# Kernel optimization log

Measured on AMD Instinct MI355X. Metric: run time of the kernel, lower is better.

## Reference

```python
import jax, jax.numpy as jnp
import numpy as np

B, S, H = 1, 1024, 2048
NH, HD = 16, 128
E, K, FI, SFI = 8, 2, 1408, 2816
EPS = 1e-6
THETA = 10000.0


def setup_inputs() -> dict:
    key = jax.random.key(0)
    ks = jax.random.split(key, 14)
    sc = 0.02
    return {
        "hidden_states": jax.random.normal(ks[0], (B, S, H), jnp.float32),
        "ln1_w": jnp.ones((H,), jnp.float32),
        "ln2_w": jnp.ones((H,), jnp.float32),
        "wq": jax.random.normal(ks[1], (H, H), jnp.float32) * sc,
        "wk": jax.random.normal(ks[2], (H, H), jnp.float32) * sc,
        "wv": jax.random.normal(ks[3], (H, H), jnp.float32) * sc,
        "wo": jax.random.normal(ks[4], (H, H), jnp.float32) * sc,
        "gate_w": jax.random.normal(ks[5], (E, H), jnp.float32) * sc,
        "expert_gate": jax.random.normal(ks[6], (E, FI, H), jnp.float32) * sc,
        "expert_up": jax.random.normal(ks[7], (E, FI, H), jnp.float32) * sc,
        "expert_down": jax.random.normal(ks[8], (E, H, FI), jnp.float32) * sc,
        "shared_gate": jax.random.normal(ks[9], (SFI, H), jnp.float32) * sc,
        "shared_up": jax.random.normal(ks[10], (SFI, H), jnp.float32) * sc,
        "shared_down": jax.random.normal(ks[11], (H, SFI), jnp.float32) * sc,
    }


def _rmsnorm(x, w):
    v = jnp.mean(x * x, axis=-1, keepdims=True)
    return x * jax.lax.rsqrt(v + EPS) * w


def _rotate_half(x):
    x1, x2 = x[..., : HD // 2], x[..., HD // 2 :]
    return jnp.concatenate((-x2, x1), axis=-1)


def _rope_cos_sin():
    inv_freq = 1.0 / (THETA ** (jnp.arange(0, HD, 2, dtype=jnp.float32) / HD))
    t = jnp.arange(S, dtype=jnp.float32)
    freqs = t[:, None] * inv_freq[None, :]          # [S, HD//2]
    emb = jnp.concatenate((freqs, freqs), axis=-1)  # [S, HD]
    return jnp.cos(emb)[None, None], jnp.sin(emb)[None, None]  # [1,1,S,HD]


def _decoder_layer(hidden_states, ln1_w, ln2_w, wq, wk, wv, wo, gate_w,
                   expert_gate, expert_up, expert_down,
                   shared_gate, shared_up, shared_down):
    # ---- self-attention ----
    residual = hidden_states
    h = _rmsnorm(hidden_states, ln1_w)
    q = (h @ wq.T).reshape(B, S, NH, HD).transpose(0, 2, 1, 3)  # [B,NH,S,HD]
    k = (h @ wk.T).reshape(B, S, NH, HD).transpose(0, 2, 1, 3)
    v = (h @ wv.T).reshape(B, S, NH, HD).transpose(0, 2, 1, 3)
    cos, sin = _rope_cos_sin()
    q = q * cos + _rotate_half(q) * sin
    k = k * cos + _rotate_half(k) * sin
    scores = jnp.einsum('bhqd,bhkd->bhqk', q, k) / jnp.sqrt(jnp.float32(HD))
    causal = jnp.tril(jnp.ones((S, S), bool))
    scores = jnp.where(causal[None, None], scores, jnp.finfo(jnp.float32).min)
    probs = jax.nn.softmax(scores, axis=-1)
    attn = jnp.einsum('bhqk,bhkd->bhqd', probs, v)
    attn = attn.transpose(0, 2, 1, 3).reshape(B, S, H)
    x = residual + attn @ wo.T

    # ---- MoE MLP ----
    residual = x
    h2 = _rmsnorm(x, ln2_w)
    flat = h2.reshape(-1, H)                       # [N,H], N=B*S
    n_tok = flat.shape[0]
    logits = flat @ gate_w.T                       # [N,E]
    gate_scores = jax.nn.softmax(logits, axis=-1)
    topk_w, topk_idx = jax.lax.top_k(gate_scores, K)
    topk_w = topk_w / (jnp.sum(topk_w, axis=-1, keepdims=True) + 1e-20)
    # dense combine weights [N,E] (zero for unrouted experts)
    combine = jnp.zeros((n_tok, E), flat.dtype).at[
        jnp.arange(n_tok)[:, None], topk_idx].add(topk_w)
    # SwiGLU per expert, dense over all experts, then weighted combine
    g = jnp.einsum('nh,efh->enf', flat, expert_gate)   # [E,N,FI]
    u = jnp.einsum('nh,efh->enf', flat, expert_up)
    act = jax.nn.silu(g) * u
    eo = jnp.einsum('enf,ehf->enh', act, expert_down)  # [E,N,H]
    routed = jnp.einsum('enh,ne->nh', eo, combine)
    # shared experts (always on)
    shared = (jax.nn.silu(flat @ shared_gate.T) * (flat @ shared_up.T)) @ shared_down.T
    return residual + (routed + shared).reshape(B, S, H)


def reference(hidden_states, ln1_w, ln2_w, wq, wk, wv, wo, gate_w,
              expert_gate, expert_up, expert_down,
              shared_gate, shared_up, shared_down):
    return _decoder_layer(hidden_states, ln1_w, ln2_w, wq, wk, wv, wo, gate_w,
                          expert_gate, expert_up, expert_down,
                          shared_gate, shared_up, shared_down)
```

## Files before the change

kernel.cpp:

```cpp
#include <hip/hip_runtime.h>
#include <hip/hip_bf16.h>


#define DI __device__ __forceinline__

typedef __attribute__((ext_vector_type(8))) short short8;
typedef __attribute__((ext_vector_type(4))) float f32x4;
using u16 = unsigned short;

struct alignas(8) U16x4 { u16 x, y, z, w; };

DI u16 f2bf(float f) {
  unsigned u = __float_as_uint(f);
  u += 0x7fffu + ((u >> 16) & 1u);
  return (u16)(u >> 16);
}
DI float bf2f(u16 h) { return __uint_as_float(((unsigned)h) << 16); }

DI void gload16(const void* g, void* l) {
  __builtin_amdgcn_global_load_lds((const __attribute__((address_space(1))) void*)g,
                                   (__attribute__((address_space(3))) void*)l, 16, 0, 0);
}


__global__ __launch_bounds__(256) void k_ropetab(float* __restrict__ tab) {
  int idx = blockIdx.x * 256 + threadIdx.x;
  int s = idx >> 6, i = idx & 63;
  double inv = pow(10000.0, -(double)(2 * i) / 128.0);
  double ang = (double)s * inv;
  tab[idx * 2 + 0] = (float)cos(ang);
  tab[idx * 2 + 1] = (float)sin(ang);
}

__global__ __launch_bounds__(256) void k_rmsnorm(const float* __restrict__ in,
                                                 const float* __restrict__ w,
                                                 float* __restrict__ outf,
                                                 u16* __restrict__ outh,
                                                 u16* __restrict__ outl) {
  const int row = blockIdx.x, t = threadIdx.x;
  const float* x = in + (size_t)row * 2048;
  float4 a = *(const float4*)&x[t * 4];
  float4 b = *(const float4*)&x[1024 + t * 4];
  float ss = a.x * a.x + a.y * a.y + a.z * a.z + a.w * a.w +
             b.x * b.x + b.y * b.y + b.z * b.z + b.w * b.w;
#pragma unroll
  for (int off = 32; off; off >>= 1) ss += __shfl_xor(ss, off);
  __shared__ float red[4];
  if ((t & 63) == 0) red[t >> 6] = ss;
  __syncthreads();
  float total = red[0] + red[1] + red[2] + red[3];
  float r = 1.0f / sqrtf(total * (1.0f / 2048.0f) + 1e-6f);
  float4 wa = *(const float4*)&w[t * 4];
  float4 wb = *(const float4*)&w[1024 + t * 4];
  float va[8] = {a.x * r * wa.x, a.y * r * wa.y, a.z * r * wa.z, a.w * r * wa.w,
                 b.x * r * wb.x, b.y * r * wb.y, b.z * r * wb.z, b.w * r * wb.w};
  if (outf) {
    *(float4*)&outf[(size_t)row * 2048 + t * 4] = make_float4(va[0], va[1], va[2], va[3]);
    *(float4*)&outf[(size_t)row * 2048 + 1024 + t * 4] = make_float4(va[4], va[5], va[6], va[7]);
  }
  if (outh) {
    U16x4 ha{f2bf(va[0]), f2bf(va[1]), f2bf(va[2]), f2bf(va[3])};
    U16x4 hb{f2bf(va[4]), f2bf(va[5]), f2bf(va[6]), f2bf(va[7])};
    *(U16x4*)&outh[(size_t)row * 2048 + t * 4] = ha;
    *(U16x4*)&outh[(size_t)row * 2048 + 1024 + t * 4] = hb;
    if (outl) {
      U16x4 la{f2bf(va[0] - bf2f(ha.x)), f2bf(va[1] - bf2f(ha.y)),
               f2bf(va[2] - bf2f(ha.z)), f2bf(va[3] - bf2f(ha.w))};
      U16x4 lb{f2bf(va[4] - bf2f(hb.x)), f2bf(va[5] - bf2f(hb.y)),
               f2bf(va[6] - bf2f(hb.z)), f2bf(va[7] - bf2f(hb.w))};
      *(U16x4*)&outl[(size_t)row * 2048 + t * 4] = la;
      *(U16x4*)&outl[(size_t)row * 2048 + 1024 + t * 4] = lb;
    }
  }
}

__global__ __launch_bounds__(256) void k_splitf(const float* __restrict__ src,
                                                u16* __restrict__ dh,
                                                u16* __restrict__ dl) {
  int idx = (blockIdx.x * 256 + threadIdx.x) * 4;
  float4 v = *(const float4*)&src[idx];
  U16x4 h{f2bf(v.x), f2bf(v.y), f2bf(v.z), f2bf(v.w)};
  U16x4 l{f2bf(v.x - bf2f(h.x)), f2bf(v.y - bf2f(h.y)),
          f2bf(v.z - bf2f(h.z)), f2bf(v.w - bf2f(h.w))};
  *(U16x4*)&dh[idx] = h;
  *(U16x4*)&dl[idx] = l;
}

__global__ __launch_bounds__(256) void k_rope(float* __restrict__ q, float* __restrict__ k,
                                              const float* __restrict__ tab) {
  int idx = blockIdx.x * 256 + threadIdx.x;
  int s = idx >> 10, rem = idx & 1023;
  int h = rem >> 6, i = rem & 63;
  size_t base = (size_t)s * 2048 + h * 128 + i;
  float c = tab[(s * 64 + i) * 2 + 0];
  float sn = tab[(s * 64 + i) * 2 + 1];
  const float qs = 0.08838834764831845f;
  float q1 = q[base], q2 = q[base + 64];
  q[base] = (q1 * c - q2 * sn) * qs;
  q[base + 64] = (q2 * c + q1 * sn) * qs;
  float k1 = k[base], k2 = k[base + 64];
  k[base] = k1 * c - k2 * sn;
  k[base + 64] = k2 * c + k1 * sn;
}

__global__ __launch_bounds__(256) void k_splitkv(
    const float* __restrict__ qf, const float* __restrict__ kf,
    const float* __restrict__ vf,
    u16* __restrict__ Qh, u16* __restrict__ Ql,
    u16* __restrict__ Kh, u16* __restrict__ Kl,
    u16* __restrict__ Vth, u16* __restrict__ Vtl) {
  int idx = (blockIdx.x * 256 + threadIdx.x) * 4;
  int s = idx >> 11, c = idx & 2047;
  float4 q4 = *(const float4*)&qf[idx];
  U16x4 qh{f2bf(q4.x), f2bf(q4.y), f2bf(q4.z), f2bf(q4.w)};
  U16x4 ql{f2bf(q4.x - bf2f(qh.x)), f2bf(q4.y - bf2f(qh.y)),
           f2bf(q4.z - bf2f(qh.z)), f2bf(q4.w - bf2f(qh.w))};
  *(U16x4*)&Qh[idx] = qh; *(U16x4*)&Ql[idx] = ql;
  float4 k4 = *(const float4*)&kf[idx];
  U16x4 kh{f2bf(k4.x), f2bf(k4.y), f2bf(k4.z), f2bf(k4.w)};
  U16x4 kl{f2bf(k4.x - bf2f(kh.x)), f2bf(k4.y - bf2f(kh.y)),
           f2bf(k4.z - bf2f(kh.z)), f2bf(k4.w - bf2f(kh.w))};
  *(U16x4*)&Kh[idx] = kh; *(U16x4*)&Kl[idx] = kl;
  float4 v4 = *(const float4*)&vf[idx];
  float vv[4] = {v4.x, v4.y, v4.z, v4.w};
#pragma unroll
  for (int i = 0; i < 4; ++i) {
    u16 hv = f2bf(vv[i]);
    u16 lv = f2bf(vv[i] - bf2f(hv));
    Vth[(size_t)(c + i) * 1024 + s] = hv;
    Vtl[(size_t)(c + i) * 1024 + s] = lv;
  }
}

DI void stage_kv(const u16* __restrict__ Khg, const u16* __restrict__ Klg,
                 const u16* __restrict__ Vhg, const u16* __restrict__ Vlg,
                 u16* lsKh, u16* lsKl, u16* lsVh, u16* lsVl,
                 int kvb, int hh, int wv, int lane) {
#pragma unroll
  for (int it = 0; it < 4; ++it) {
    const int ebase = it * 2048 + wv * 512;
    const int eo = ebase + lane * 8;
    {
      const int rr = eo >> 7, cg = (eo >> 3) & 15;
      const size_t src = (size_t)(kvb + rr) * 2048 + hh * 128 + ((cg ^ (rr & 7)) << 3);
      gload16(Khg + src, lsKh + ebase);
      gload16(Klg + src, lsKl + ebase);
    }
    {
      const int rr = eo >> 6, cg = (eo >> 3) & 7;
      const size_t src = (size_t)(hh * 128 + rr) * 1024 + kvb + ((cg ^ (rr & 7)) << 3);
      gload16(Vhg + src, lsVh + ebase);
      gload16(Vlg + src, lsVl + ebase);
    }
  }
}

__global__ __launch_bounds__(256) void k_attn_tile(
    const u16* __restrict__ Qh, const u16* __restrict__ Ql,
    const u16* __restrict__ Khg, const u16* __restrict__ Klg,
    const u16* __restrict__ Vhg, const u16* __restrict__ Vlg,
    u16* __restrict__ atth, u16* __restrict__ attl) {
  __shared__ u16 lsKh[2][8192], lsKl[2][8192], lsVh[2][8192], lsVl[2][8192];
  __shared__ u16 Plh[4][16][72], Pll[4][16][72];
  const int hh = blockIdx.y;
  const int qb = blockIdx.x * 64;
  const int tid = threadIdx.x, lane = tid & 63, wv = tid >> 6;
  const int l15 = lane & 15, grp = lane >> 4;
  u16(*plh)[72] = Plh[wv];
  u16(*pll)[72] = Pll[wv];
  const int q_glob = qb + wv * 16 + l15;
  const int tend = blockIdx.x + 1;

  short8 qfh[4], qfl[4];
  const size_t qbase = (size_t)q_glob * 2048 + hh * 128;
#pragma unroll
  for (int c = 0; c < 4; ++c) {
    qfh[c] = *(const short8*)&Qh[qbase + c * 32 + grp * 8];
    qfl[c] = *(const short8*)&Ql[qbase + c * 32 + grp * 8];
  }
  f32x4 oacc[8];
#pragma unroll
  for (int dc = 0; dc < 8; ++dc) oacc[dc] = 0.f;
  float m_run = -1e30f, l_run = 0.f;

  int cur = 0;
  stage_kv(Khg, Klg, Vhg, Vlg, lsKh[0], lsKl[0], lsVh[0], lsVl[0], 0, hh, wv, lane);
  __syncthreads();

  for (int kt = 0; kt < tend; ++kt) {
    const int kvb = kt * 64;
    if (kt + 1 < tend)
      stage_kv(Khg, Klg, Vhg, Vlg, lsKh[cur ^ 1], lsKl[cur ^ 1], lsVh[cur ^ 1],
               lsVl[cur ^ 1], kvb + 64, hh, wv, lane);
    const u16* kh = lsKh[cur];
    const u16* kl = lsKl[cur];
    const u16* vh = lsVh[cur];
    const u16* vl = lsVl[cur];

    f32x4 s4[4];
#pragma unroll
    for (int sub = 0; sub < 4; ++sub) {
      f32x4 a = {0.f, 0.f, 0.f, 0.f};
      const int kr = sub * 16 + l15;
      const int sw = kr & 7;
#pragma unroll
      for (int c = 0; c < 4; ++c) {
        const int off = kr * 128 + ((((c << 2) | grp) ^ sw) << 3);
        short8 khf = *(const short8*)&kh[off];
        short8 klf = *(const short8*)&kl[off];
        a = __builtin_amdgcn_mfma_f32_16x16x32_bf16(khf, qfh[c], a, 0, 0, 0);
        a = __builtin_amdgcn_mfma_f32_16x16x32_bf16(klf, qfh[c], a, 0, 0, 0);
        a = __builtin_amdgcn_mfma_f32_16x16x32_bf16(khf, qfl[c], a, 0, 0, 0);
      }
      s4[sub] = a;
    }
    if (kt == tend - 1) {
#pragma unroll
      for (int sub = 0; sub < 4; ++sub)
#pragma unroll
        for (int r = 0; r < 4; ++r) {
          int kv = kvb + sub * 16 + grp * 4 + r;
          if (kv > q_glob) s4[sub][r] = -1e30f;
        }
    }
    float tmax = s4[0][0];
#pragma unroll
    for (int sub = 0; sub < 4; ++sub)
#pragma unroll
      for (int r = 0; r < 4; ++r) tmax = fmaxf(tmax, s4[sub][r]);
    tmax = fmaxf(tmax, __shfl_xor(tmax, 16));
    tmax = fmaxf(tmax, __shfl_xor(tmax, 32));
    float mnew = fmaxf(m_run, tmax);
    float scale = expf(m_run - mnew);
    float p[16], lsum = 0.f;
#pragma unroll
    for (int sub = 0; sub < 4; ++sub)
#pragma unroll
      for (int r = 0; r < 4; ++r) {
        float pe = expf(s4[sub][r] - mnew);
        p[sub * 4 + r] = pe;
        lsum += pe;
      }
    lsum += __shfl_xor(lsum, 16);
    lsum += __shfl_xor(lsum, 32);
    l_run = l_run * scale + lsum;
    m_run = mnew;
#pragma unroll
    for (int dc = 0; dc < 8; ++dc) oacc[dc] *= scale;
#pragma unroll
    for (int sub = 0; sub < 4; ++sub)
#pragma unroll
      for (int rp = 0; rp < 2; ++rp) {
        int i0 = sub * 4 + rp * 2;
        u16 h0 = f2bf(p[i0]), h1 = f2bf(p[i0 + 1]);
        u16 lo0 = f2bf(p[i0] - bf2f(h0)), lo1 = f2bf(p[i0 + 1] - bf2f(h1));
        int kvoff = sub * 16 + grp * 4 + rp * 2;
        *(unsigned*)&plh[l15][kvoff] = (unsigned)h0 | ((unsigned)h1 << 16);
        *(unsigned*)&pll[l15][kvoff] = (unsigned)lo0 | ((unsigned)lo1 << 16);
      }
    short8 phf[2], plf[2];
#pragma unroll
    for (int ks = 0; ks < 2; ++ks) {
      phf[ks] = *(const short8*)&plh[l15][ks * 32 + grp * 8];
      plf[ks] = *(const short8*)&pll[l15][ks * 32 + grp * 8];
    }
#pragma unroll
    for (int dc = 0; dc < 8; ++dc) {
      const int dr = dc * 16 + l15;
      const int sw = dr & 7;
      f32x4 acc = oacc[dc];
#pragma unroll
      for (int ks = 0; ks < 2; ++ks) {
        const int voff = dr * 64 + ((((ks << 2) | grp) ^ sw) << 3);
        short8 vhf = *(const short8*)&vh[voff];
        short8 vlf = *(const short8*)&vl[voff];
        acc = __builtin_amdgcn_mfma_f32_16x16x32_bf16(vhf, phf[ks], acc, 0, 0, 0);
        acc = __builtin_amdgcn_mfma_f32_16x16x32_bf16(vlf, phf[ks], acc, 0, 0, 0);
        acc = __builtin_amdgcn_mfma_f32_16x16x32_bf16(vhf, plf[ks], acc, 0, 0, 0);
      }
      oacc[dc] = acc;
    }
    __syncthreads();
    cur ^= 1;
  }
  float inv = 1.0f / l_run;
#pragma unroll
  for (int dc = 0; dc < 8; ++dc)
#pragma unroll
    for (int rp = 0; rp < 2; ++rp) {
      float v0 = oacc[dc][rp * 2] * inv;
      float v1 = oacc[dc][rp * 2 + 1] * inv;
      u16 h0 = f2bf(v0), h1 = f2bf(v1);
      u16 lo0 = f2bf(v0 - bf2f(h0)), lo1 = f2bf(v1 - bf2f(h1));
      size_t o = (size_t)q_glob * 2048 + hh * 128 + dc * 16 + grp * 4 + rp * 2;
      *(unsigned*)&atth[o] = (unsigned)h0 | ((unsigned)h1 << 16);
      *(unsigned*)&attl[o] = (unsigned)lo0 | ((unsigned)lo1 << 16);
    }
}

__global__ __launch_bounds__(256) void k_router(const float* __restrict__ h2f,
                                                const float* __restrict__ gw,
                                                int2* __restrict__ tidx,
                                                float2* __restrict__ twgt) {
  const int tok = blockIdx.x;
  const float* hrow = h2f + (size_t)tok * 2048;
  float part[8];
#pragma unroll
  for (int e = 0; e < 8; ++e) part[e] = 0.f;
  for (int j = 0; j < 8; ++j) {
    int p = j * 256 + threadIdx.x;
    float hv = hrow[p];
#pragma unroll
    for (int e = 0; e < 8; ++e) part[e] += hv * gw[e * 2048 + p];
  }
#pragma unroll
  for (int e = 0; e < 8; ++e)
#pragma unroll
    for (int off = 32; off; off >>= 1) part[e] += __shfl_xor(part[e], off);
  __shared__ float red[4][8];
  int wv = threadIdx.x >> 6, lane = threadIdx.x & 63;
  if (lane == 0) {
#pragma unroll
    for (int e = 0; e < 8; ++e) red[wv][e] = part[e];
  }
  __syncthreads();
  if (threadIdx.x == 0) {
    float lg[8];
#pragma unroll
    for (int e = 0; e < 8; ++e) lg[e] = red[0][e] + red[1][e] + red[2][e] + red[3][e];
    float m = lg[0];
#pragma unroll
    for (int e = 1; e < 8; ++e) m = fmaxf(m, lg[e]);
    float ex[8], s = 0.f;
#pragma unroll
    for (int e = 0; e < 8; ++e) { ex[e] = expf(lg[e] - m); s += ex[e]; }
#pragma unroll
    for (int e = 0; e < 8; ++e) ex[e] /= s;
    int i1 = 0;
#pragma unroll
    for (int e = 1; e < 8; ++e) if (ex[e] > ex[i1]) i1 = e;
    int i2 = (i1 == 0) ? 1 : 0;
#pragma unroll
    for (int e = 0; e < 8; ++e) if (e != i1 && ex[e] > ex[i2]) i2 = e;
    float s2 = ex[i1] + ex[i2] + 1e-20f;
    tidx[tok] = make_int2(i1, i2);
    twgt[tok] = make_float2(ex[i1] / s2, ex[i2] / s2);
  }
}

__global__ __launch_bounds__(64) void k_scan(const int2* __restrict__ tidx,
                                             const float2* __restrict__ twgt,
                                             int* __restrict__ meta,
                                             int* __restrict__ toklist,
                                             float* __restrict__ slotw,
                                             int* __restrict__ slots) {
  const int lane = threadIdx.x;
  int base = 0;
  for (int e = 0; e < 8; ++e) {
    int cnt = 0;
    for (int c = 0; c < 16; ++c) {
      const int tok = c * 64 + lane;
      int2 my = tidx[tok];
      int f1 = (my.x == e), f2 = (my.y == e);
      int flag = f1 | f2;
      unsigned long long m = __ballot(flag);
      if (flag) {
        float2 w = twgt[tok];
        int rank = (int)__popcll(m & ((1ull << lane) - 1ull));
        int s = base + cnt + rank;
        toklist[s] = tok;
        slotw[s] = f1 ? w.x : w.y;
        slots[tok * 2 + (f1 ? 0 : 1)] = s;
      }
      cnt += (int)__popcll(m);
    }
    if (lane == 0) { meta[e] = base; meta[9 + e] = cnt; }
    const int padded = ((cnt + 127) >> 7) << 7;
    for (int s = cnt + lane; s < padded; s += 64) {
      toklist[base + s] = 0;
      slotw[base + s] = 0.f;
    }
    base += padded;
  }
  if (lane == 0) meta[8] = base;
}


DI void stageA_bf16(const u16* __restrict__ A, size_t lda, int row0, int k0,
                    u16* lsA, int tid) {
  const int lane = tid & 63, wv = tid >> 6;
#pragma unroll
  for (int it = 0; it < 2; ++it) {
    const int ebase = it * 2048 + wv * 512;
    const int eo = ebase + lane * 8;
    const int rr = eo >> 5, cc = eo & 31;
    gload16(A + (size_t)(row0 + rr) * lda + k0 + cc, lsA + ebase);
  }
}
template <int NJ>
DI void loadB_regs(const float* __restrict__ B, size_t ldb, int row0, int k0,
                   int tid, float4* r) {
#pragma unroll
  for (int j = 0; j < NJ; ++j) {
    const int eo = (j * 256 + tid) * 4;
    const int rr = eo >> 5, cc = eo & 31;
    r[j] = *(const float4*)(B + (size_t)(row0 + rr) * ldb + k0 + cc);
  }
}
template <int NJ>
DI void writeB_lds(u16* lsB, int tid, const float4* r) {
#pragma unroll
  for (int j = 0; j < NJ; ++j) {
    const int eo = (j * 256 + tid) * 4;
    U16x4 hv{f2bf(r[j].x), f2bf(r[j].y), f2bf(r[j].z), f2bf(r[j].w)};
    *(U16x4*)&lsB[eo] = hv;
  }
}

__global__ __launch_bounds__(256) void k_gemm_bf16split(
    const u16* __restrict__ Ah, const u16* __restrict__ Al,
    const u16* __restrict__ Bh0, const u16* __restrict__ Bl0,
    const u16* __restrict__ Bh1, const u16* __restrict__ Bl1,
    const u16* __restrict__ Bh2, const u16* __restrict__ Bl2,
    float* __restrict__ C0, float* __restrict__ C1, float* __restrict__ C2,
    const float* __restrict__ resid) {
  __shared__ u16 lsAh[4096], lsAl[4096], lsBh[4096], lsBl[4096];
  const int z = blockIdx.z;
  const u16* Bh = (z == 0) ? Bh0 : (z == 1) ? Bh1 : Bh2;
  const u16* Bl = (z == 0) ? Bl0 : (z == 1) ? Bl1 : Bl2;
  float* Cm = (z == 0) ? C0 : (z == 1) ? C1 : C2;
  const int tid = threadIdx.x, lane = tid & 63, wv = tid >> 6;
  const int wr = (wv >> 1) * 64, wc = (wv & 1) * 64;
  const int fr = lane & 15, fg = lane >> 4;
  const int row0 = blockIdx.x * 128, col0 = blockIdx.y * 128;
  f32x4 acc[4][4];
#pragma unroll
  for (int i = 0; i < 4; ++i)
#pragma unroll
    for (int j = 0; j < 4; ++j) acc[i][j] = 0.f;

  for (int kt = 0; kt < 64; ++kt) {
    const int k0 = kt * 32;
    stageA_bf16(Ah, 2048, row0, k0, lsAh, tid);
    stageA_bf16(Al, 2048, row0, k0, lsAl, tid);
    stageA_bf16(Bh, 2048, col0, k0, lsBh, tid);
    stageA_bf16(Bl, 2048, col0, k0, lsBl, tid);
    __syncthreads();
    short8 ah[4], al[4], bh[4], bl[4];
#pragma unroll
    for (int mi = 0; mi < 4; ++mi) {
      const int off = (wr + mi * 16 + fr) * 32 + fg * 8;
      ah[mi] = *(const short8*)&lsAh[off];
      al[mi] = *(const short8*)&lsAl[off];
    }
#pragma unroll
    for (int ni = 0; ni < 4; ++ni) {
      const int off = (wc + ni * 16 + fr) * 32 + fg * 8;
      bh[ni] = *(const short8*)&lsBh[off];
      bl[ni] = *(const short8*)&lsBl[off];
    }
#pragma unroll
    for (int mi = 0; mi < 4; ++mi)
#pragma unroll
      for (int ni = 0; ni < 4; ++ni) {
        f32x4 c = acc[mi][ni];
        c = __builtin_amdgcn_mfma_f32_16x16x32_bf16(al[mi], bh[ni], c, 0, 0, 0);
        c = __builtin_amdgcn_mfma_f32_16x16x32_bf16(ah[mi], bl[ni], c, 0, 0, 0);
        c = __builtin_amdgcn_mfma_f32_16x16x32_bf16(ah[mi], bh[ni], c, 0, 0, 0);
        acc[mi][ni] = c;
      }
    __syncthreads();
  }
  const bool hasres = (resid != nullptr);
#pragma unroll
  for (int mi = 0; mi < 4; ++mi)
#pragma unroll
    for (int ni = 0; ni < 4; ++ni)
#pragma unroll
      for (int qq = 0; qq < 4; ++qq) {
        const int row = row0 + wr + mi * 16 + fg * 4 + qq;
        const int col = col0 + wc + ni * 16 + fr;
        float val = acc[mi][ni][qq];
        if (hasres) val += resid[(size_t)row * 2048 + col];
        Cm[(size_t)row * 2048 + col] = val;
      }
}

DI int tile_to_expert(const int* meta, int t) {
  int e = 0;
  while (e < 7 && t >= (meta[e + 1] >> 7)) ++e;
  return e;
}

__global__ __launch_bounds__(256) void k_dual_all(
    const u16* __restrict__ h2b, const float* __restrict__ eg,
    const float* __restrict__ eu, const float* __restrict__ sg,
    const float* __restrict__ su, const int* __restrict__ meta,
    const int* __restrict__ toklist, const float* __restrict__ slotw,
    u16* __restrict__ act, u16* __restrict__ acts) {
  const int bid = blockIdx.x;
  const bool isShared = bid >= 528;
  __shared__ int toks[128];
  __shared__ u16 lsA[2][4096], lsG[2][2048], lsU[2][2048];
  const int tid = threadIdx.x, lane = tid & 63, wv = tid >> 6;
  const int wr = (wv >> 1) * 64, wc = (wv & 1) * 32;
  const int fr = lane & 15, fg = lane >> 4;

  int n0, e = 0, off_e = 0, cnt_e = 0, rtile = 0;
  const float *Bg, *Bu;
  if (isShared) {
    const int b2 = bid - 528;
    rtile = b2 / 44;
    n0 = (b2 % 44) * 64;
    Bg = sg;
    Bu = su;
    if (tid < 128) toks[tid] = rtile * 128 + tid;
  } else {
    const int t = bid / 22;
    if (t >= (meta[8] >> 7)) return;
    n0 = (bid % 22) * 64;
    e = tile_to_expert(meta, t);
    off_e = meta[e];
    cnt_e = meta[9 + e];
    rtile = t - (off_e >> 7);
    Bg = eg + (size_t)e * 1408 * 2048;
    Bu = eu + (size_t)e * 1408 * 2048;
    if (tid < 128) toks[tid] = toklist[off_e + rtile * 128 + tid] & 1023;
  }
  f32x4 ag[4][2], au[4][2];
#pragma unroll
  for (int i = 0; i < 4; ++i)
#pragma unroll
    for (int j = 0; j < 2; ++j) { ag[i][j] = 0.f; au[i][j] = 0.f; }
  __syncthreads();

  auto stageAg = [&](u16* dst, int k0) {
#pragma unroll
    for (int it = 0; it < 2; ++it) {
      const int ebase = it * 2048 + wv * 512;
      const int eo = ebase + lane * 8;
      const int rr = eo >> 5, cc = eo & 31;
      gload16(h2b + (size_t)toks[rr] * 2048 + k0 + cc, dst + ebase);
    }
  };

  float4 gpre[2], upre[2];
  stageAg(lsA[0], 0);
  loadB_regs<2>(Bg, 2048, n0, 0, tid, gpre);
  loadB_regs<2>(Bu, 2048, n0, 0, tid, upre);
  writeB_lds<2>(lsG[0], tid, gpre);
  writeB_lds<2>(lsU[0], tid, upre);
  __syncthreads();

  int cur = 0;
  for (int kt = 0; kt < 64; ++kt) {
    const int k1 = (kt + 1) * 32;
    const bool pf = (kt + 1 < 64);
    if (pf) {
      stageAg(lsA[cur ^ 1], k1);
      loadB_regs<2>(Bg, 2048, n0, k1, tid, gpre);
      loadB_regs<2>(Bu, 2048, n0, k1, tid, upre);
    }
    short8 af[4], gf[2], uf[2];
#pragma unroll
    for (int mi = 0; mi < 4; ++mi)
      af[mi] = *(const short8*)&lsA[cur][(wr + mi * 16 + fr) * 32 + fg * 8];
#pragma unroll
    for (int ni = 0; ni < 2; ++ni) {
      const int off = (wc + ni * 16 + fr) * 32 + fg * 8;
      gf[ni] = *(const short8*)&lsG[cur][off];
      uf[ni] = *(const short8*)&lsU[cur][off];
    }
#pragma unroll
    for (int mi = 0; mi < 4; ++mi)
#pragma unroll
      for (int ni = 0; ni < 2; ++ni) {
        ag[mi][ni] = __builtin_amdgcn_mfma_f32_16x16x32_bf16(af[mi], gf[ni], ag[mi][ni], 0, 0, 0);
        au[mi][ni] = __builtin_amdgcn_mfma_f32_16x16x32_bf16(af[mi], uf[ni], au[mi][ni], 0, 0, 0);
      }
    if (pf) {
      writeB_lds<2>(lsG[cur ^ 1], tid, gpre);
      writeB_lds<2>(lsU[cur ^ 1], tid, upre);
    }
    __syncthreads();
    cur ^= 1;
  }
#pragma unroll
  for (int mi = 0; mi < 4; ++mi)
#pragma unroll
    for (int ni = 0; ni < 2; ++ni)
#pragma unroll
      for (int qq = 0; qq < 4; ++qq) {
        const int r = wr + mi * 16 + fg * 4 + qq;
        const int col = n0 + wc + ni * 16 + fr;
        float g = ag[mi][ni][qq], u = au[mi][ni][qq];
        float a = g / (1.0f + expf(-g)) * u;
        if (isShared) {
          acts[(size_t)(rtile * 128 + r) * 2816 + col] = f2bf(a);
        } else {
          const int rowInE = rtile * 128 + r;
          if (rowInE < cnt_e)
            act[(size_t)(off_e + rowInE) * 1408 + col] = f2bf(a * slotw[off_e + rowInE]);
        }
      }
}

__global__ __launch_bounds__(256) void k_down_all(
    const u16* __restrict__ act, const float* __restrict__ ed,
    const u16* __restrict__ acts, const float* __restrict__ sd,
    const int* __restrict__ meta, float* __restrict__ dwn,
    float* __restrict__ shd) {
  __shared__ u16 lsA[2][4096], lsB[2][4096];
  const int bid = blockIdx.x;
  const int tid = threadIdx.x, lane = tid & 63, wv = tid >> 6;
  const int fr = lane & 15, fg = lane >> 4;
  if (bid < 384) {
    const int t = bid >> 4;
    if (t >= (meta[8] >> 7)) return;
    const int col0 = (bid & 15) * 128;
    const int e = tile_to_expert(meta, t);
    const int off_e = meta[e];
    const int rtile = t - (off_e >> 7);
    const int wr = (wv >> 1) * 64, wc = (wv & 1) * 64;
    const u16* Ab = act + (size_t)off_e * 1408;
    const float* Bb = ed + (size_t)e * 2048 * 1408;
    f32x4 acc[4][4];
#pragma unroll
    for (int i = 0; i < 4; ++i)
#pragma unroll
      for (int j = 0; j < 4; ++j) acc[i][j] = 0.f;
    float4 bpre[4];
    stageA_bf16(Ab, 1408, rtile * 128, 0, lsA[0], tid);
    loadB_regs<4>(Bb, 1408, col0, 0, tid, bpre);
    writeB_lds<4>(lsB[0], tid, bpre);
    __syncthreads();
    int cur = 0;
    for (int kt = 0; kt < 44; ++kt) {
      const int k1 = (kt + 1) * 32;
      const bool pf = (kt + 1 < 44);
      if (pf) {
        stageA_bf16(Ab, 1408, rtile * 128, k1, lsA[cur ^ 1], tid);
        loadB_regs<4>(Bb, 1408, col0, k1, tid, bpre);
      }
      short8 af[4], bf_[4];
#pragma unroll
      for (int mi = 0; mi < 4; ++mi)
        af[mi] = *(const short8*)&lsA[cur][(wr + mi * 16 + fr) * 32 + fg * 8];
#pragma unroll
      for (int ni = 0; ni < 4; ++ni)
        bf_[ni] = *(const short8*)&lsB[cur][(wc + ni * 16 + fr) * 32 + fg * 8];
#pragma unroll
      for (int mi = 0; mi < 4; ++mi)
#pragma unroll
        for (int ni = 0; ni < 4; ++ni)
          acc[mi][ni] = __builtin_amdgcn_mfma_f32_16x16x32_bf16(af[mi], bf_[ni], acc[mi][ni], 0, 0, 0);
      if (pf) writeB_lds<4>(lsB[cur ^ 1], tid, bpre);
      __syncthreads();
      cur ^= 1;
    }
#pragma unroll
    for (int mi = 0; mi < 4; ++mi)
#pragma unroll
      for (int ni = 0; ni < 4; ++ni)
#pragma unroll
        for (int qq = 0; qq < 4; ++qq) {
          const int r = wr + mi * 16 + fg * 4 + qq;
          const int col = col0 + wc + ni * 16 + fr;
          dwn[(size_t)(off_e + rtile * 128 + r) * 2048 + col] = acc[mi][ni][qq];
        }
  } else {
    const int b2 = bid - 384;
    const int row0 = (b2 >> 5) * 128;
    const int col0 = (b2 & 31) * 64;
    const int wr = (wv >> 1) * 64, wc = (wv & 1) * 32;
    f32x4 acc[4][2];
#pragma unroll
    for (int i = 0; i < 4; ++i)
#pragma unroll
      for (int j = 0; j < 2; ++j) acc[i][j] = 0.f;
    float4 bpre[2];
    stageA_bf16(acts, 2816, row0, 0, lsA[0], tid);
    loadB_regs<2>(sd, 2816, col0, 0, tid, bpre);
    writeB_lds<2>(lsB[0], tid, bpre);
    __syncthreads();
    int cur = 0;
    for (int kt = 0; kt < 88; ++kt) {
      const int k1 = (kt + 1) * 32;
      const bool pf = (kt + 1 < 88);
      if (pf) {
        stageA_bf16(acts, 2816, row0, k1, lsA[cur ^ 1], tid);
        loadB_regs<2>(sd, 2816, col0, k1, tid, bpre);
      }
      short8 af[4], bf_[2];
#pragma unroll
      for (int mi = 0; mi < 4; ++mi)
        af[mi] = *(const short8*)&lsA[cur][(wr + mi * 16 + fr) * 32 + fg * 8];
#pragma unroll
      for (int ni = 0; ni < 2; ++ni)
        bf_[ni] = *(const short8*)&lsB[cur][(wc + ni * 16 + fr) * 32 + fg * 8];
#pragma unroll
      for (int mi = 0; mi < 4; ++mi)
#pragma unroll
        for (int ni = 0; ni < 2; ++ni)
          acc[mi][ni] = __builtin_amdgcn_mfma_f32_16x16x32_bf16(af[mi], bf_[ni], acc[mi][ni], 0, 0, 0);
      if (pf) writeB_lds<2>(lsB[cur ^ 1], tid, bpre);
      __syncthreads();
      cur ^= 1;
    }
#pragma unroll
    for (int mi = 0; mi < 4; ++mi)
#pragma unroll
      for (int ni = 0; ni < 2; ++ni)
#pragma unroll
        for (int qq = 0; qq < 4; ++qq) {
          const int row = row0 + wr + mi * 16 + fg * 4 + qq;
          const int col = col0 + wc + ni * 16 + fr;
          shd[(size_t)row * 2048 + col] = acc[mi][ni][qq];
        }
  }
}

__global__ __launch_bounds__(256) void k_combine(
    const float* __restrict__ shd, const float* __restrict__ x,
    const float* __restrict__ dwn, const int* __restrict__ slots,
    float* __restrict__ outp) {
  const int i4 = (blockIdx.x * 256 + threadIdx.x) * 4;
  const int row = i4 >> 11, col = i4 & 2047;
  const int s0 = slots[row * 2], s1 = slots[row * 2 + 1];
  float4 a = *(const float4*)&shd[i4];
  float4 b = *(const float4*)&x[i4];
  float4 c = *(const float4*)&dwn[(size_t)s0 * 2048 + col];
  float4 d = *(const float4*)&dwn[(size_t)s1 * 2048 + col];
  float4 o;
  o.x = a.x + b.x + c.x + d.x;
  o.y = a.y + b.y + c.y + d.y;
  o.z = a.z + b.z + c.z + d.z;
  o.w = a.w + b.w + c.w + d.w;
  *(float4*)&outp[i4] = o;
}


extern "C" void kernel_launch(void* const* d_in, const int* in_sizes, int n_in,
                              void* d_out, int out_size, void* d_ws, size_t ws_size,
                              hipStream_t stream) {
  (void)in_sizes; (void)n_in; (void)out_size; (void)ws_size;
  const float* hidden = (const float*)d_in[0];
  const float* ln1 = (const float*)d_in[1];
  const float* ln2 = (const float*)d_in[2];
  const float* wq = (const float*)d_in[3];
  const float* wk = (const float*)d_in[4];
  const float* wvw = (const float*)d_in[5];
  const float* wo = (const float*)d_in[6];
  const float* gw = (const float*)d_in[7];
  const float* eg = (const float*)d_in[8];
  const float* eu = (const float*)d_in[9];
  const float* ed = (const float*)d_in[10];
  const float* sg = (const float*)d_in[11];
  const float* su = (const float*)d_in[12];
  const float* sd = (const float*)d_in[13];
  float* out = (float*)d_out;
  char* ws = (char*)d_ws;

  const size_t KB = 1ull << 10, MB = 1ull << 20;
  float* tab = (float*)(ws + 0);
  int2* tidx = (int2*)(ws + 512 * KB);
  float2* twgt = (float2*)(ws + 520 * KB);
  int* meta = (int*)(ws + 528 * KB);
  int* tokl = (int*)(ws + 532 * KB);
  float* slw = (float*)(ws + 544 * KB);
  int* slots = (int*)(ws + 556 * KB);
  u16* hnh = (u16*)(ws + 1 * MB);
  u16* hnl = (u16*)(ws + 5 * MB);
  u16* wqh = (u16*)(ws + 9 * MB);
  u16* wql = (u16*)(ws + 17 * MB);
  u16* wkh = (u16*)(ws + 25 * MB);
  u16* wkl = (u16*)(ws + 33 * MB);
  u16* wvh = (u16*)(ws + 41 * MB);
  u16* wvl = (u16*)(ws + 49 * MB);
  u16* woh = (u16*)(ws + 57 * MB);
  u16* wol = (u16*)(ws + 65 * MB);
  float* qf = (float*)(ws + 73 * MB);
  float* kf = (float*)(ws + 81 * MB);
  float* vf = (float*)(ws + 89 * MB);
  u16* Qh = (u16*)(ws + 9 * MB);
  u16* Ql = (u16*)(ws + 13 * MB);
  u16* Kh = (u16*)(ws + 17 * MB);
  u16* Kl = (u16*)(ws + 21 * MB);
  u16* Vth = (u16*)(ws + 25 * MB);
  u16* Vtl = (u16*)(ws + 29 * MB);
  u16* atth = (u16*)(ws + 33 * MB);
  u16* attl = (u16*)(ws + 37 * MB);
  float* xf = (float*)(ws + 41 * MB);
  float* h2f = (float*)(ws + 49 * MB);
  u16* h2b = (u16*)(ws + 1 * MB);
  u16* act = (u16*)(ws + 73 * MB);
  u16* acts = (u16*)(ws + 82 * MB);
  float* dwn = (float*)(ws + 9 * MB);
  float* shd = (float*)(ws + 33 * MB);

  k_ropetab<<<256, 256, 0, stream>>>(tab);
  k_rmsnorm<<<1024, 256, 0, stream>>>(hidden, ln1, nullptr, hnh, hnl);
  k_splitf<<<4096, 256, 0, stream>>>(wq, wqh, wql);
  k_splitf<<<4096, 256, 0, stream>>>(wk, wkh, wkl);
  k_splitf<<<4096, 256, 0, stream>>>(wvw, wvh, wvl);
  k_splitf<<<4096, 256, 0, stream>>>(wo, woh, wol);
  k_gemm_bf16split<<<dim3(8, 16, 3), 256, 0, stream>>>(
      hnh, hnl, wqh, wql, wkh, wkl, wvh, wvl, qf, kf, vf, nullptr);
  k_rope<<<4096, 256, 0, stream>>>(qf, kf, tab);
  k_splitkv<<<2048, 256, 0, stream>>>(qf, kf, vf, Qh, Ql, Kh, Kl, Vth, Vtl);
  k_attn_tile<<<dim3(16, 16), 256, 0, stream>>>(Qh, Ql, Kh, Kl, Vth, Vtl, atth, attl);
  k_gemm_bf16split<<<dim3(8, 16, 1), 256, 0, stream>>>(
      atth, attl, woh, wol, woh, wol, woh, wol, xf, xf, xf, hidden);
  k_rmsnorm<<<1024, 256, 0, stream>>>(xf, ln2, h2f, h2b, nullptr);
  k_router<<<1024, 256, 0, stream>>>(h2f, gw, tidx, twgt);
  k_scan<<<1, 64, 0, stream>>>(tidx, twgt, meta, tokl, slw, slots);
  k_dual_all<<<880, 256, 0, stream>>>(h2b, eg, eu, sg, su, meta, tokl, slw, act, acts);
  k_down_all<<<640, 256, 0, stream>>>(act, ed, acts, sd, meta, dwn, shd);
  k_combine<<<2048, 256, 0, stream>>>(shd, xf, dwn, slots, out);
}
```

Measured before the change: 590.1 us.

## Remap MoE GEMM block order for XCD locality, hoist addresses, merge weight splits

Block indices in the expert gate/up and down kernels are remapped so that each group of blocks (blockIdx mod 8, likely meant to match the XCDs) works on the same weight columns across row tiles. This is meant to improve L2 reuse of the fp32 weight streams. Per-iteration address arithmetic is hoisted into precomputed pointers. The bf16 conversion of weight tiles now uses a cheaper round-half-up pack that drops round-to-nearest-even, so results can differ slightly. The four weight-split launches are merged into one kernel.

Result: slower. 635.8 us (+7.7%).

```diff
diff --git a/kernel.cpp b/kernel.cpp
--- a/kernel.cpp
+++ b/kernel.cpp
@@ -16,6 +16,11 @@
   return (u16)(u >> 16);
 }
 DI float bf2f(u16 h) { return __uint_as_float(((unsigned)h) << 16); }
+DI unsigned pack2(float f0, float f1) {
+  unsigned a = __float_as_uint(f0) + 0x8000u;
+  unsigned b = __float_as_uint(f1) + 0x8000u;
+  return (a >> 16) | (b & 0xffff0000u);
+}
 
 DI void gload16(const void* g, void* l) {
   __builtin_amdgcn_global_load_lds((const __attribute__((address_space(1))) void*)g,
@@ -74,10 +79,17 @@
   }
 }
 
-__global__ __launch_bounds__(256) void k_splitf(const float* __restrict__ src,
-                                                u16* __restrict__ dh,
-                                                u16* __restrict__ dl) {
-  int idx = (blockIdx.x * 256 + threadIdx.x) * 4;
+__global__ __launch_bounds__(256) void k_splitf4(
+    const float* __restrict__ s0, const float* __restrict__ s1,
+    const float* __restrict__ s2, const float* __restrict__ s3,
+    u16* __restrict__ h0, u16* __restrict__ h1, u16* __restrict__ h2,
+    u16* __restrict__ h3, u16* __restrict__ l0, u16* __restrict__ l1,
+    u16* __restrict__ l2, u16* __restrict__ l3) {
+  const int which = blockIdx.x >> 12;
+  const int idx = ((blockIdx.x & 4095) * 256 + threadIdx.x) * 4;
+  const float* src = (which == 0) ? s0 : (which == 1) ? s1 : (which == 2) ? s2 : s3;
+  u16* dh = (which == 0) ? h0 : (which == 1) ? h1 : (which == 2) ? h2 : h3;
+  u16* dl = (which == 0) ? l0 : (which == 1) ? l1 : (which == 2) ? l2 : l3;
   float4 v = *(const float4*)&src[idx];
   U16x4 h{f2bf(v.x), f2bf(v.y), f2bf(v.z), f2bf(v.w)};
   U16x4 l{f2bf(v.x - bf2f(h.x)), f2bf(v.y - bf2f(h.y)),
@@ -397,25 +409,6 @@
     gload16(A + (size_t)(row0 + rr) * lda + k0 + cc, lsA + ebase);
   }
 }
-template <int NJ>
-DI void loadB_regs(const float* __restrict__ B, size_t ldb, int row0, int k0,
-                   int tid, float4* r) {
-#pragma unroll
-  for (int j = 0; j < NJ; ++j) {
-    const int eo = (j * 256 + tid) * 4;
-    const int rr = eo >> 5, cc = eo & 31;
-    r[j] = *(const float4*)(B + (size_t)(row0 + rr) * ldb + k0 + cc);
-  }
-}
-template <int NJ>
-DI void writeB_lds(u16* lsB, int tid, const float4* r) {
-#pragma unroll
-  for (int j = 0; j < NJ; ++j) {
-    const int eo = (j * 256 + tid) * 4;
-    U16x4 hv{f2bf(r[j].x), f2bf(r[j].y), f2bf(r[j].z), f2bf(r[j].w)};
-    *(U16x4*)&lsB[eo] = hv;
-  }
-}
 
 __global__ __launch_bounds__(256) void k_gemm_bf16split(
     const u16* __restrict__ Ah, const u16* __restrict__ Al,
@@ -498,28 +491,28 @@
     const float* __restrict__ su, const int* __restrict__ meta,
     const int* __restrict__ toklist, const float* __restrict__ slotw,
     u16* __restrict__ act, u16* __restrict__ acts) {
-  const int bid = blockIdx.x;
-  const bool isShared = bid >= 528;
+  const int wid = ((blockIdx.x & 7) * 110) + (blockIdx.x >> 3);
+  const bool isShared = wid >= 528;
   __shared__ int toks[128];
   __shared__ u16 lsA[2][4096], lsG[2][2048], lsU[2][2048];
   const int tid = threadIdx.x, lane = tid & 63, wv = tid >> 6;
   const int wr = (wv >> 1) * 64, wc = (wv & 1) * 32;
   const int fr = lane & 15, fg = lane >> 4;
 
-  int n0, e = 0, off_e = 0, cnt_e = 0, rtile = 0;
+  int n0, off_e = 0, cnt_e = 0, rtile = 0;
   const float *Bg, *Bu;
   if (isShared) {
-    const int b2 = bid - 528;
-    rtile = b2 / 44;
-    n0 = (b2 % 44) * 64;
+    const int b2 = wid - 528;
+    rtile = b2 & 7;
+    n0 = (b2 >> 3) * 64;
     Bg = sg;
     Bu = su;
     if (tid < 128) toks[tid] = rtile * 128 + tid;
   } else {
-    const int t = bid / 22;
+    const int t = wid % 24;
+    n0 = (wid / 24) * 64;
     if (t >= (meta[8] >> 7)) return;
-    n0 = (bid % 22) * 64;
-    e = tile_to_expert(meta, t);
+    const int e = tile_to_expert(meta, t);
     off_e = meta[e];
     cnt_e = meta[9 + e];
     rtile = t - (off_e >> 7);
@@ -534,22 +527,29 @@
     for (int j = 0; j < 2; ++j) { ag[i][j] = 0.f; au[i][j] = 0.f; }
   __syncthreads();
 
-  auto stageAg = [&](u16* dst, int k0) {
-#pragma unroll
-    for (int it = 0; it < 2; ++it) {
-      const int ebase = it * 2048 + wv * 512;
-      const int eo = ebase + lane * 8;
-      const int rr = eo >> 5, cc = eo & 31;
-      gload16(h2b + (size_t)toks[rr] * 2048 + k0 + cc, dst + ebase);
-    }
-  };
-
-  float4 gpre[2], upre[2];
-  stageAg(lsA[0], 0);
-  loadB_regs<2>(Bg, 2048, n0, 0, tid, gpre);
-  loadB_regs<2>(Bu, 2048, n0, 0, tid, upre);
-  writeB_lds<2>(lsG[0], tid, gpre);
-  writeB_lds<2>(lsU[0], tid, upre);
+  const int ebase0 = wv * 512, ebase1 = 2048 + wv * 512;
+  const int eoA0 = ebase0 + lane * 8, eoA1 = ebase1 + lane * 8;
+  const u16* aS0 = h2b + (size_t)toks[eoA0 >> 5] * 2048 + (eoA0 & 31);
+  const u16* aS1 = h2b + (size_t)toks[eoA1 >> 5] * 2048 + (eoA1 & 31);
+  const int eoB0 = tid * 4, eoB1 = (256 + tid) * 4;
+  const float* gB0 = Bg + (size_t)(n0 + (eoB0 >> 5)) * 2048 + (eoB0 & 31);
+  const float* gB1 = Bg + (size_t)(n0 + (eoB1 >> 5)) * 2048 + (eoB1 & 31);
+  const float* uB0 = Bu + (size_t)(n0 + (eoB0 >> 5)) * 2048 + (eoB0 & 31);
+  const float* uB1 = Bu + (size_t)(n0 + (eoB1 >> 5)) * 2048 + (eoB1 & 31);
+
+  float4 g0, g1, u0, u1;
+  gload16(aS0, lsA[0] + ebase0);
+  gload16(aS1, lsA[0] + ebase1);
+  g0 = *(const float4*)gB0; g1 = *(const float4*)gB1;
+  u0 = *(const float4*)uB0; u1 = *(const float4*)uB1;
+  *(unsigned*)&lsG[0][eoB0] = pack2(g0.x, g0.y);
+  *(unsigned*)&lsG[0][eoB0 + 2] = pack2(g0.z, g0.w);
+  *(unsigned*)&lsG[0][eoB1] = pack2(g1.x, g1.y);
+  *(unsigned*)&lsG[0][eoB1 + 2] = pack2(g1.z, g1.w);
+  *(unsigned*)&lsU[0][eoB0] = pack2(u0.x, u0.y);
+  *(unsigned*)&lsU[0][eoB0 + 2] = pack2(u0.z, u0.w);
+  *(unsigned*)&lsU[0][eoB1] = pack2(u1.x, u1.y);
+  *(unsigned*)&lsU[0][eoB1 + 2] = pack2(u1.z, u1.w);
   __syncthreads();
 
   int cur = 0;
@@ -557,9 +557,12 @@
     const int k1 = (kt + 1) * 32;
     const bool pf = (kt + 1 < 64);
     if (pf) {
-      stageAg(lsA[cur ^ 1], k1);
-      loadB_regs<2>(Bg, 2048, n0, k1, tid, gpre);
-      loadB_regs<2>(Bu, 2048, n0, k1, tid, upre);
+      gload16(aS0 + k1, lsA[cur ^ 1] + ebase0);
+      gload16(aS1 + k1, lsA[cur ^ 1] + ebase1);
+      g0 = *(const float4*)(gB0 + k1);
+      g1 = *(const float4*)(gB1 + k1);
+      u0 = *(const float4*)(uB0 + k1);
+      u1 = *(const float4*)(uB1 + k1);
     }
     short8 af[4], gf[2], uf[2];
 #pragma unroll
@@ -579,8 +582,16 @@
         au[mi][ni] = __builtin_amdgcn_mfma_f32_16x16x32_bf16(af[mi], uf[ni], au[mi][ni], 0, 0, 0);
       }
     if (pf) {
-      writeB_lds<2>(lsG[cur ^ 1], tid, gpre);
-      writeB_lds<2>(lsU[cur ^ 1], tid, upre);
+      u16* lg = lsG[cur ^ 1];
+      u16* lu = lsU[cur ^ 1];
+      *(unsigned*)&lg[eoB0] = pack2(g0.x, g0.y);
+      *(unsigned*)&lg[eoB0 + 2] = pack2(g0.z, g0.w);
+      *(unsigned*)&lg[eoB1] = pack2(g1.x, g1.y);
+      *(unsigned*)&lg[eoB1 + 2] = pack2(g1.z, g1.w);
+      *(unsigned*)&lu[eoB0] = pack2(u0.x, u0.y);
+      *(unsigned*)&lu[eoB0 + 2] = pack2(u0.z, u0.w);
+      *(unsigned*)&lu[eoB1] = pack2(u1.x, u1.y);
+      *(unsigned*)&lu[eoB1 + 2] = pack2(u1.z, u1.w);
     }
     __syncthreads();
     cur ^= 1;
@@ -611,36 +622,55 @@
     const int* __restrict__ meta, float* __restrict__ dwn,
     float* __restrict__ shd) {
   __shared__ u16 lsA[2][4096], lsB[2][4096];
-  const int bid = blockIdx.x;
+  const int wid = ((blockIdx.x & 7) * 80) + (blockIdx.x >> 3);
   const int tid = threadIdx.x, lane = tid & 63, wv = tid >> 6;
   const int fr = lane & 15, fg = lane >> 4;
-  if (bid < 384) {
-    const int t = bid >> 4;
+  const int ebase0 = wv * 512, ebase1 = 2048 + wv * 512;
+  const int eoA0 = ebase0 + lane * 8, eoA1 = ebase1 + lane * 8;
+  if (wid < 384) {
+    const int t = wid % 24;
+    const int col0 = (wid / 24) * 128;
     if (t >= (meta[8] >> 7)) return;
-    const int col0 = (bid & 15) * 128;
     const int e = tile_to_expert(meta, t);
     const int off_e = meta[e];
     const int rtile = t - (off_e >> 7);
     const int wr = (wv >> 1) * 64, wc = (wv & 1) * 64;
     const u16* Ab = act + (size_t)off_e * 1408;
     const float* Bb = ed + (size_t)e * 2048 * 1408;
+    const u16* aS0 = Ab + (size_t)(rtile * 128 + (eoA0 >> 5)) * 1408 + (eoA0 & 31);
+    const u16* aS1 = Ab + (size_t)(rtile * 128 + (eoA1 >> 5)) * 1408 + (eoA1 & 31);
+    const float* bB[4];
+    int eoB[4];
+#pragma unroll
+    for (int j = 0; j < 4; ++j) {
+      eoB[j] = (j * 256 + tid) * 4;
+      bB[j] = Bb + (size_t)(col0 + (eoB[j] >> 5)) * 1408 + (eoB[j] & 31);
+    }
     f32x4 acc[4][4];
 #pragma unroll
     for (int i = 0; i < 4; ++i)
 #pragma unroll
       for (int j = 0; j < 4; ++j) acc[i][j] = 0.f;
-    float4 bpre[4];
-    stageA_bf16(Ab, 1408, rtile * 128, 0, lsA[0], tid);
-    loadB_regs<4>(Bb, 1408, col0, 0, tid, bpre);
-    writeB_lds<4>(lsB[0], tid, bpre);
+    float4 bp[4];
+    gload16(aS0, lsA[0] + ebase0);
+    gload16(aS1, lsA[0] + ebase1);
+#pragma unroll
+    for (int j = 0; j < 4; ++j) bp[j] = *(const float4*)bB[j];
+#pragma unroll
+    for (int j = 0; j < 4; ++j) {
+      *(unsigned*)&lsB[0][eoB[j]] = pack2(bp[j].x, bp[j].y);
+      *(unsigned*)&lsB[0][eoB[j] + 2] = pack2(bp[j].z, bp[j].w);
+    }
     __syncthreads();
     int cur = 0;
     for (int kt = 0; kt < 44; ++kt) {
       const int k1 = (kt + 1) * 32;
       const bool pf = (kt + 1 < 44);
       if (pf) {
-        stageA_bf16(Ab, 1408, rtile * 128, k1, lsA[cur ^ 1], tid);
-        loadB_regs<4>(Bb, 1408, col0, k1, tid, bpre);
+        gload16(aS0 + k1, lsA[cur ^ 1] + ebase0);
+        gload16(aS1 + k1, lsA[cur ^ 1] + ebase1);
+#pragma unroll
+        for (int j = 0; j < 4; ++j) bp[j] = *(const float4*)(bB[j] + k1);
       }
       short8 af[4], bf_[4];
 #pragma unroll
@@ -654,7 +684,14 @@
 #pragma unroll
         for (int ni = 0; ni < 4; ++ni)
           acc[mi][ni] = __builtin_amdgcn_mfma_f32_16x16x32_bf16(af[mi], bf_[ni], acc[mi][ni], 0, 0, 0);
-      if (pf) writeB_lds<4>(lsB[cur ^ 1], tid, bpre);
+      if (pf) {
+        u16* lb = lsB[cur ^ 1];
+#pragma unroll
+        for (int j = 0; j < 4; ++j) {
+          *(unsigned*)&lb[eoB[j]] = pack2(bp[j].x, bp[j].y);
+          *(unsigned*)&lb[eoB[j] + 2] = pack2(bp[j].z, bp[j].w);
+        }
+      }
       __syncthreads();
       cur ^= 1;
     }
@@ -669,27 +706,44 @@
           dwn[(size_t)(off_e + rtile * 128 + r) * 2048 + col] = acc[mi][ni][qq];
         }
   } else {
-    const int b2 = bid - 384;
-    const int row0 = (b2 >> 5) * 128;
-    const int col0 = (b2 & 31) * 64;
+    const int b2 = wid - 384;
+    const int row0 = (b2 & 7) * 128;
+    const int col0 = (b2 >> 3) * 64;
     const int wr = (wv >> 1) * 64, wc = (wv & 1) * 32;
+    const u16* aS0 = acts + (size_t)(row0 + (eoA0 >> 5)) * 2816 + (eoA0 & 31);
+    const u16* aS1 = acts + (size_t)(row0 + (eoA1 >> 5)) * 2816 + (eoA1 & 31);
+    const float* bB[2];
+    int eoB[2];
+#pragma unroll
+    for (int j = 0; j < 2; ++j) {
+      eoB[j] = (j * 256 + tid) * 4;
+      bB[j] = sd + (size_t)(col0 + (eoB[j] >> 5)) * 2816 + (eoB[j] & 31);
+    }
     f32x4 acc[4][2];
 #pragma unroll
     for (int i = 0; i < 4; ++i)
 #pragma unroll
       for (int j = 0; j < 2; ++j) acc[i][j] = 0.f;
-    float4 bpre[2];
-    stageA_bf16(acts, 2816, row0, 0, lsA[0], tid);
-    loadB_regs<2>(sd, 2816, col0, 0, tid, bpre);
-    writeB_lds<2>(lsB[0], tid, bpre);
+    float4 bp[2];
+    gload16(aS0, lsA[0] + ebase0);
+    gload16(aS1, lsA[0] + ebase1);
+#pragma unroll
+    for (int j = 0; j < 2; ++j) bp[j] = *(const float4*)bB[j];
+#pragma unroll
+    for (int j = 0; j < 2; ++j) {
+      *(unsigned*)&lsB[0][eoB[j]] = pack2(bp[j].x, bp[j].y);
+      *(unsigned*)&lsB[0][eoB[j] + 2] = pack2(bp[j].z, bp[j].w);
+    }
     __syncthreads();
     int cur = 0;
     for (int kt = 0; kt < 88; ++kt) {
       const int k1 = (kt + 1) * 32;
       const bool pf = (kt + 1 < 88);
       if (pf) {
-        stageA_bf16(acts, 2816, row0, k1, lsA[cur ^ 1], tid);
-        loadB_regs<2>(sd, 2816, col0, k1, tid, bpre);
+        gload16(aS0 + k1, lsA[cur ^ 1] + ebase0);
+        gload16(aS1 + k1, lsA[cur ^ 1] + ebase1);
+#pragma unroll
+        for (int j = 0; j < 2; ++j) bp[j] = *(const float4*)(bB[j] + k1);
       }
       short8 af[4], bf_[2];
 #pragma unroll
@@ -703,7 +757,14 @@
 #pragma unroll
         for (int ni = 0; ni < 2; ++ni)
           acc[mi][ni] = __builtin_amdgcn_mfma_f32_16x16x32_bf16(af[mi], bf_[ni], acc[mi][ni], 0, 0, 0);
-      if (pf) writeB_lds<2>(lsB[cur ^ 1], tid, bpre);
+      if (pf) {
+        u16* lb = lsB[cur ^ 1];
+#pragma unroll
+        for (int j = 0; j < 2; ++j) {
+          *(unsigned*)&lb[eoB[j]] = pack2(bp[j].x, bp[j].y);
+          *(unsigned*)&lb[eoB[j] + 2] = pack2(bp[j].z, bp[j].w);
+        }
+      }
       __syncthreads();
       cur ^= 1;
     }
@@ -800,10 +861,8 @@
 
   k_ropetab<<<256, 256, 0, stream>>>(tab);
   k_rmsnorm<<<1024, 256, 0, stream>>>(hidden, ln1, nullptr, hnh, hnl);
-  k_splitf<<<4096, 256, 0, stream>>>(wq, wqh, wql);
-  k_splitf<<<4096, 256, 0, stream>>>(wk, wkh, wkl);
-  k_splitf<<<4096, 256, 0, stream>>>(wvw, wvh, wvl);
-  k_splitf<<<4096, 256, 0, stream>>>(wo, woh, wol);
+  k_splitf4<<<16384, 256, 0, stream>>>(wq, wk, wvw, wo, wqh, wkh, wvh, woh,
+                                       wql, wkl, wvl, wol);
   k_gemm_bf16split<<<dim3(8, 16, 3), 256, 0, stream>>>(
       hnh, hnl, wqh, wql, wkh, wkl, wvh, wvl, qf, kf, vf, nullptr);
   k_rope<<<4096, 256, 0, stream>>>(qf, kf, tab);
```
